# Performance work log

Measured on AMD Instinct MI355X. Metric: run time of the kernel, lower is better.

The kernel has to match this reference:

```python
import jax, jax.numpy as jnp
import numpy as np

B, S, H = 1, 4096, 2048
HQ, HKV, D = 8, 4, 256
WIN = 1024          # sliding window
SOFTCAP = 50.0      # attn logit softcapping
EPS = 1e-6          # rms_norm_eps
ROPE_THETA = 10000.0


def setup_inputs() -> dict:
    key = jax.random.key(0)
    ks = jax.random.split(key, 6)
    hidden_states = jax.random.normal(ks[0], (B, S, H), dtype=jnp.float32)
    # RoPE cos/sin tables, shape [B, S, D]
    inv_freq = 1.0 / (ROPE_THETA ** (jnp.arange(0, D, 2, dtype=jnp.float32) / D))
    pos = jnp.arange(S, dtype=jnp.float32)
    freqs = pos[:, None] * inv_freq[None, :]          # [S, D/2]
    emb = jnp.concatenate([freqs, freqs], axis=-1)    # [S, D]
    cos = jnp.broadcast_to(jnp.cos(emb)[None], (B, S, D)).astype(jnp.float32)
    sin = jnp.broadcast_to(jnp.sin(emb)[None], (B, S, D)).astype(jnp.float32)
    qpos = jnp.arange(S)[:, None]
    kpos = jnp.arange(S)[None, :]
    diff = qpos - kpos
    allowed = (diff >= 0) & (diff < WIN)
    attention_mask = jnp.where(allowed, 0.0, -1e9).astype(jnp.float32)[None, None]
    attention_mask = jnp.broadcast_to(attention_mask, (B, 1, S, S))
    w_scale = 0.02
    Wq = jax.random.normal(ks[1], (HQ * D, H), dtype=jnp.float32) * w_scale
    Wk = jax.random.normal(ks[2], (HKV * D, H), dtype=jnp.float32) * w_scale
    Wv = jax.random.normal(ks[3], (HKV * D, H), dtype=jnp.float32) * w_scale
    Wo = jax.random.normal(ks[4], (H, HQ * D), dtype=jnp.float32) * w_scale
    q_norm_w = jnp.ones((D,), dtype=jnp.float32)
    k_norm_w = jnp.ones((D,), dtype=jnp.float32)
    return {"hidden_states": hidden_states, "cos": cos, "sin": sin,
            "attention_mask": attention_mask, "Wq": Wq, "Wk": Wk, "Wv": Wv,
            "Wo": Wo, "q_norm_w": q_norm_w, "k_norm_w": k_norm_w}


def _rms_norm(x, weight=None):
    # Gemma4 RMSNorm in fp32: x * rsqrt(mean(x^2) + eps) [* weight]
    ms = jnp.mean(x * x, axis=-1, keepdims=True) + EPS
    y = x * jax.lax.rsqrt(ms)
    return y * weight if weight is not None else y


def _rope(x, cos, sin):
    # x: [B,S,Hn,D]; cos/sin: [B,S,D] -> unsqueeze at dim 2
    x1, x2 = jnp.split(x, 2, axis=-1)
    rot = jnp.concatenate([-x2, x1], axis=-1)
    return x * cos[:, :, None, :] + rot * sin[:, :, None, :]


def reference(hidden_states, cos, sin, attention_mask, Wq, Wk, Wv, Wo, q_norm_w, k_norm_w):
    n_rep = HQ // HKV
    q = (hidden_states @ Wq.T).reshape(B, S, HQ, D)     # [B,S,HQ,D]
    q = _rms_norm(q, q_norm_w)
    q = _rope(q, cos, sin).transpose(0, 2, 1, 3)        # [B,HQ,S,D]
    k = (hidden_states @ Wk.T).reshape(B, S, HKV, D)
    k = _rms_norm(k, k_norm_w)
    k = _rope(k, cos, sin).transpose(0, 2, 1, 3)        # [B,HKV,S,D]
    v = (hidden_states @ Wv.T).reshape(B, S, HKV, D)
    v = _rms_norm(v).transpose(0, 2, 1, 3)              # [B,HKV,S,D]
    # repeat_kv (GQA)
    k = jnp.repeat(k, n_rep, axis=1)                    # [B,HQ,S,D]
    v = jnp.repeat(v, n_rep, axis=1)
    scores = jnp.einsum('bhqd,bhkd->bhqk', q, k)        # scaling = 1.0
    scores = jnp.tanh(scores / SOFTCAP) * SOFTCAP       # softcap
    scores = scores + attention_mask
    attn = jax.nn.softmax(scores.astype(jnp.float32), axis=-1).astype(q.dtype)
    out = jnp.einsum('bhqk,bhkd->bhqd', attn, v)        # [B,HQ,S,D]
    out = out.transpose(0, 2, 1, 3).reshape(B, S, HQ * D)
    return out @ Wo.T                                   # [B,S,H]
```

## Files before the change

kernel.cpp:

```cpp
#include <hip/hip_runtime.h>

#define S_LEN 4096
#define HID   2048
#define NHQ   8
#define NKV   4
#define DHEAD 256
#define WIN   1024

typedef __attribute__((ext_vector_type(4))) float     floatx4;
typedef __attribute__((ext_vector_type(8))) _Float16  halfx8;
typedef __attribute__((ext_vector_type(8))) __bf16    bf16x8;

__device__ __forceinline__ unsigned short f2h(float f){
  union { _Float16 h; unsigned short u; } cv; cv.h = (_Float16)f; return cv.u;
}
__device__ __forceinline__ float h2f(unsigned short u){
  union { unsigned short u; _Float16 h; } cv; cv.u = u; return (float)cv.h;
}
__device__ __forceinline__ unsigned short f2bf(float f){
  unsigned int u = __float_as_uint(f);
  u += 0x7FFFu + ((u >> 16) & 1u);
  return (unsigned short)(u >> 16);
}

__device__ __forceinline__ void gld_lds16(const void* g, void* l){
  __builtin_amdgcn_global_load_lds((const __attribute__((address_space(1))) void*)g,
                                   (__attribute__((address_space(3))) void*)l, 16, 0, 0);
}

__global__ __launch_bounds__(256) void cvt_all(const float* __restrict__ hs,
                                               const float* __restrict__ Wq,
                                               const float* __restrict__ Wk,
                                               const float* __restrict__ Wv,
                                               const float* __restrict__ Wo,
                                               unsigned short* __restrict__ h_h,
                                               unsigned short* __restrict__ w_qkv,
                                               unsigned short* __restrict__ wo){
  int bid = blockIdx.x;
  const float* src;
  unsigned short* dst;
  size_t i;
  if (bid < 8192){
    i = ((size_t)bid * 256 + threadIdx.x) * 4;
    src = hs + i; dst = h_h + i;
  } else if (bid < 16384){
    i = ((size_t)(bid - 8192) * 256 + threadIdx.x) * 4;
    int row = (int)(i >> 11), col = (int)(i & 2047);
    src = ((row < 2048) ? (Wq + ((size_t)row << 11))
         : (row < 3072) ? (Wk + ((size_t)(row - 2048) << 11))
                        : (Wv + ((size_t)(row - 3072) << 11))) + col;
    dst = w_qkv + i;
  } else {
    i = ((size_t)(bid - 16384) * 256 + threadIdx.x) * 4;
    src = Wo + i; dst = wo + i;
  }
  float4 v = *(const float4*)src;
  *(ushort4*)dst = make_ushort4(f2h(v.x), f2h(v.y), f2h(v.z), f2h(v.w));
}

template<int OUT_F32>
__global__ __launch_bounds__(256, 2) void gemm_ht(const unsigned short* __restrict__ A,
                                                  const unsigned short* __restrict__ B,
                                                  void* __restrict__ Cv,
                                                  int ldC, int K){
  __shared__ __align__(16) unsigned short As[128 * 32];
  __shared__ __align__(16) unsigned short Bs[128 * 32];
  const int t = threadIdx.x, w = t >> 6, lane = t & 63;
  const int quad = lane >> 4, l15 = lane & 15;
  const int l2 = lane >> 2, g8 = (lane & 3) * 8;
  const int wm = w >> 1, wn = w & 1;
  const int bm0 = blockIdx.y * 128, bn0 = blockIdx.x * 128;

  const floatx4 zf = {0.f, 0.f, 0.f, 0.f};
  floatx4 acc[4][4];
#pragma unroll
  for (int mi = 0; mi < 4; ++mi)
#pragma unroll
    for (int ni = 0; ni < 4; ++ni) acc[mi][ni] = zf;

  for (int k0 = 0; k0 < K; k0 += 32){
#pragma unroll
    for (int j = 0; j < 2; ++j){
      int ch  = j * 4 + w;
      int row = ch * 16 + l2;
      gld_lds16(A + (size_t)(bm0 + row) * K + k0 + g8, &As[ch * 512]);
      gld_lds16(B + (size_t)(bn0 + row) * K + k0 + g8, &Bs[ch * 512]);
    }
    __syncthreads();
    halfx8 af[4], bf[4];
#pragma unroll
    for (int mi = 0; mi < 4; ++mi) af[mi] = *(const halfx8*)&As[(wm*64 + mi*16 + l15)*32 + quad*8];
#pragma unroll
    for (int ni = 0; ni < 4; ++ni) bf[ni] = *(const halfx8*)&Bs[(wn*64 + ni*16 + l15)*32 + quad*8];
#pragma unroll
    for (int mi = 0; mi < 4; ++mi)
#pragma unroll
      for (int ni = 0; ni < 4; ++ni)
        acc[mi][ni] = __builtin_amdgcn_mfma_f32_16x16x32_f16(af[mi], bf[ni], acc[mi][ni], 0, 0, 0);
    __syncthreads();
  }
#pragma unroll
  for (int mi = 0; mi < 4; ++mi)
#pragma unroll
    for (int ni = 0; ni < 4; ++ni)
#pragma unroll
      for (int r = 0; r < 4; ++r){
        int m = bm0 + wm*64 + mi*16 + quad*4 + r;
        int n = bn0 + wn*64 + ni*16 + l15;
        float v = acc[mi][ni][r];
        if (OUT_F32) ((float*)Cv)[(size_t)m * ldC + n] = v;
        else         ((unsigned short*)Cv)[(size_t)m * ldC + n] = f2h(v);
      }
}

__global__ __launch_bounds__(256) void qkv_post(const unsigned short* __restrict__ qkvh,
                                                const float* __restrict__ cosb,
                                                const float* __restrict__ sinb,
                                                const float* __restrict__ qnw,
                                                const float* __restrict__ knw,
                                                unsigned short* __restrict__ Qf,
                                                unsigned short* __restrict__ Kf,
                                                unsigned short* __restrict__ Vf){
  int gw   = blockIdx.x * 4 + (threadIdx.x >> 6);
  int lane = threadIdx.x & 63;
  int hh = gw & 15, s = gw >> 4;
  int colbase = (hh < 8) ? hh * 256 : (hh < 12 ? 2048 + (hh - 8) * 256 : 3072 + (hh - 12) * 256);

  ushort4 raw = *(const ushort4*)(qkvh + (size_t)s * 4096 + colbase + lane * 4);
  float x0 = h2f(raw.x), x1 = h2f(raw.y), x2 = h2f(raw.z), x3 = h2f(raw.w);
  float ss = x0*x0 + x1*x1 + x2*x2 + x3*x3;
#pragma unroll
  for (int off = 32; off; off >>= 1) ss += __shfl_xor(ss, off);
  float inv = rsqrtf(ss * (1.0f / 256.0f) + 1e-6f);

  if (hh < 12){
    const float* wp = (hh < 8) ? qnw : knw;
    float4 wv = *(const float4*)(wp + lane * 4);
    float y[4] = { x0*inv*wv.x, x1*inv*wv.y, x2*inv*wv.z, x3*inv*wv.w };
    float4 cv = *(const float4*)(cosb + (size_t)s * 256 + lane * 4);
    float4 sv = *(const float4*)(sinb + (size_t)s * 256 + lane * 4);
    float cj[4] = {cv.x, cv.y, cv.z, cv.w};
    float sj[4] = {sv.x, sv.y, sv.z, sv.w};
    unsigned short oh[4];
#pragma unroll
    for (int j = 0; j < 4; ++j){
      float oth = __shfl_xor(y[j], 32);
      float rot = (lane < 32) ? -oth : oth;
      oh[j] = f2h(y[j] * cj[j] + rot * sj[j]);
    }
    ushort4 r = make_ushort4(oh[0], oh[1], oh[2], oh[3]);
    if (hh < 8) *(ushort4*)(Qf + (size_t)(hh       * S_LEN + s) * DHEAD + lane * 4) = r;
    else        *(ushort4*)(Kf + (size_t)((hh - 8) * S_LEN + s) * DHEAD + lane * 4) = r;
  } else {
    ushort4 r = make_ushort4(f2bf(x0*inv), f2bf(x1*inv), f2bf(x2*inv), f2bf(x3*inv));
    *(ushort4*)(Vf + (size_t)((hh - 12) * S_LEN + s) * DHEAD + lane * 4) = r;
  }
}

__global__ __launch_bounds__(256) void transpose_v(const unsigned short* __restrict__ v,
                                                   unsigned short* __restrict__ vt){
  __shared__ unsigned short tile[64][68];
  int kv = blockIdx.z, d0 = blockIdx.x * 64, s0 = blockIdx.y * 64;
  int t = threadIdx.x;
  int r = t >> 4, c4 = (t & 15) * 4;
#pragma unroll
  for (int i = 0; i < 4; ++i){
    int row = r + i * 16;
    ushort4 xx = *(const ushort4*)(v + (size_t)(kv * S_LEN + s0 + row) * DHEAD + d0 + c4);
    tile[row][c4] = xx.x; tile[row][c4+1] = xx.y; tile[row][c4+2] = xx.z; tile[row][c4+3] = xx.w;
  }
  __syncthreads();
#pragma unroll
  for (int i = 0; i < 4; ++i){
    int dr = r + i * 16;
    ushort4 yy = make_ushort4(tile[c4][dr], tile[c4+1][dr], tile[c4+2][dr], tile[c4+3][dr]);
    *(ushort4*)(vt + (size_t)(kv * DHEAD + d0 + dr) * S_LEN + s0 + c4) = yy;
  }
}

__global__ __launch_bounds__(256, 2) void attn_win(const unsigned short* __restrict__ Qg,
                                                   const unsigned short* __restrict__ Kg,
                                                   const unsigned short* __restrict__ Vt,
                                                   unsigned short* __restrict__ Og){
  __shared__ __align__(16) unsigned short Ks[2][8 * 32 * 32];
  __shared__ __align__(16) unsigned short Vts[2][256 * 32];
  __shared__ __align__(16) unsigned short Pb[4][16 * 40];

  const int bid = blockIdx.x;
  const int h = bid & 7, kv = h >> 1;
  const int q0 = (bid >> 3) * 64;
  const int t = threadIdx.x, w = t >> 6, lane = t & 63;
  const int quad = lane >> 4, l15 = lane & 15;
  const int l2 = lane >> 2;
  const int gsw = (((lane & 3) ^ ((l2 >> 1) & 3)) << 3);
  const int qsw = ((quad ^ ((l15 >> 1) & 3)) << 3);
  const int qw0 = q0 + w * 16;

  halfx8 qf[8];
#pragma unroll
  for (int c = 0; c < 8; ++c)
    qf[c] = *(const halfx8*)(Qg + (size_t)(h * S_LEN + qw0 + l15) * DHEAD + c*32 + quad*8);

  const floatx4 zf = {0.f, 0.f, 0.f, 0.f};
  floatx4 oacc[16];
#pragma unroll
  for (int dt = 0; dt < 16; ++dt) oacc[dt] = zf;
  float l_part[4] = {0.f, 0.f, 0.f, 0.f};

  int kt_lo = q0 / 32 - 32; if (kt_lo < 0) kt_lo = 0;
  int kt_hi = q0 / 32 + 1;

  const size_t kbase = (size_t)kv * S_LEN * DHEAD;
  const size_t vbase = (size_t)kv * DHEAD * S_LEN;

#define STAGE(KT, B)                                                              \
  {                                                                               \
    const int key0_ = (KT) * 32;                                                  \
    _Pragma("unroll")                                                             \
    for (int j = 0; j < 4; ++j){                                                  \
      int ch = j * 4 + w;                                                         \
      int krow = (ch & 1) * 16 + l2;                                              \
      int cb = ch >> 1;                                                           \
      gld_lds16(Kg + kbase + (size_t)(key0_ + krow) * DHEAD + cb * 32 + gsw,      \
                &Ks[B][ch * 512]);                                                \
      int drow = ch * 16 + l2;                                                    \
      gld_lds16(Vt + vbase + (size_t)drow * S_LEN + key0_ + gsw,                  \
                &Vts[B][ch * 512]);                                               \
    }                                                                             \
  }

  STAGE(kt_lo, 0);

  for (int kt = kt_lo; kt <= kt_hi; ++kt){
    const int cur = (kt - kt_lo) & 1;
    __syncthreads();
    if (kt < kt_hi) STAGE(kt + 1, cur ^ 1);

    const int key0 = kt * 32;
    if (key0 <= qw0 + 15 && key0 + 31 >= qw0 - (WIN - 1)){
      floatx4 sc[2];
      sc[0] = zf; sc[1] = zf;
      __builtin_amdgcn_s_setprio(1);
#pragma unroll
      for (int c = 0; c < 8; ++c){
#pragma unroll
        for (int nt = 0; nt < 2; ++nt){
          halfx8 kf = *(const halfx8*)&Ks[cur][c * 1024 + (nt*16 + l15) * 32 + qsw];
          sc[nt] = __builtin_amdgcn_mfma_f32_16x16x32_f16(qf[c], kf, sc[nt], 0, 0, 0);
        }
      }
      __builtin_amdgcn_s_setprio(0);
      const bool tfull = (key0 + 31 <= qw0) && (qw0 + 15 - key0 < WIN);
#pragma unroll
      for (int nt = 0; nt < 2; ++nt)
#pragma unroll
        for (int r = 0; r < 4; ++r){
          float v = sc[nt][r];
          float e  = __builtin_amdgcn_exp2f(v * 0.0577078016f);
          float tt = __builtin_amdgcn_rcpf(e + 1.0f);
          float p  = __builtin_amdgcn_exp2f(fmaf(tt, -144.26950408f, 28.8539008f));
          if (!tfull){
            int qi = qw0 + quad*4 + r;
            int ki = key0 + nt*16 + l15;
            p = ((ki <= qi) && (qi - ki < WIN)) ? p : 0.0f;
          }
          l_part[r] += p;
          Pb[w][(quad*4 + r) * 40 + nt*16 + l15] = f2bf(p);
        }
      bf16x8 pf = *(const bf16x8*)&Pb[w][l15 * 40 + quad * 8];
      __builtin_amdgcn_s_setprio(1);
#pragma unroll
      for (int dt = 0; dt < 16; ++dt){
        bf16x8 vf = *(const bf16x8*)&Vts[cur][(dt*16 + l15) * 32 + qsw];
        oacc[dt] = __builtin_amdgcn_mfma_f32_16x16x32_bf16(pf, vf, oacc[dt], 0, 0, 0);
      }
      __builtin_amdgcn_s_setprio(0);
    }
  }
#undef STAGE

#pragma unroll
  for (int r = 0; r < 4; ++r){
    float l = l_part[r];
    l += __shfl_xor(l, 1);
    l += __shfl_xor(l, 2);
    l += __shfl_xor(l, 4);
    l += __shfl_xor(l, 8);
    float rl = 1.0f / l;
    int srow = qw0 + quad*4 + r;
#pragma unroll
    for (int dt = 0; dt < 16; ++dt)
      Og[(size_t)srow * (NHQ * DHEAD) + h * DHEAD + dt*16 + l15] = f2h(oacc[dt][r] * rl);
  }
}

extern "C" void kernel_launch(void* const* d_in, const int* in_sizes, int n_in,
                              void* d_out, int out_size, void* d_ws, size_t ws_size,
                              hipStream_t stream){
  const float* hs   = (const float*)d_in[0];
  const float* cosb = (const float*)d_in[1];
  const float* sinb = (const float*)d_in[2];
  const float* Wq   = (const float*)d_in[4];
  const float* Wk   = (const float*)d_in[5];
  const float* Wv   = (const float*)d_in[6];
  const float* Wo   = (const float*)d_in[7];
  const float* qnw  = (const float*)d_in[8];
  const float* knw  = (const float*)d_in[9];
  float* out = (float*)d_out;

  const size_t MB = 1024ull * 1024ull;
  char* ws = (char*)d_ws;
  unsigned short* h_h   = (unsigned short*)(ws);
  unsigned short* w_qkv = (unsigned short*)(ws + 16 * MB);
  unsigned short* wo    = (unsigned short*)(ws + 32 * MB);
  unsigned short* qkvh  = (unsigned short*)(ws + 40 * MB);
  unsigned short* Qf    = (unsigned short*)(ws);
  unsigned short* Kf    = (unsigned short*)(ws + 16 * MB);
  unsigned short* Vf    = (unsigned short*)(ws + 24 * MB);
  unsigned short* vt    = (unsigned short*)(ws + 40 * MB);
  unsigned short* ob    = (unsigned short*)(ws + 48 * MB);

  cvt_all<<<20480, 256, 0, stream>>>(hs, Wq, Wk, Wv, Wo, h_h, w_qkv, wo);

  gemm_ht<0><<<dim3(32, 32), 256, 0, stream>>>(h_h, w_qkv, qkvh, 4096, 2048);

  qkv_post<<<16384, 256, 0, stream>>>(qkvh, cosb, sinb, qnw, knw, Qf, Kf, Vf);
  transpose_v<<<dim3(4, 64, 4), 256, 0, stream>>>(Vf, vt);

  attn_win<<<512, 256, 0, stream>>>(Qf, Kf, vt, ob);

  gemm_ht<1><<<dim3(16, 32), 256, 0, stream>>>(ob, wo, out, 2048, 2048);
}
```

Measured before the change: 395.5 us.

## Replace QKV projection GEMM with 256x256 tile, 4-stage LDS pipelined kernel

Adds a dedicated QKV projection GEMM that uses 256x256 block tiles with 512 threads and a 4-deep ring of LDS stages. The stages are filled by direct global-to-LDS loads with a swizzled layout, and the block index is remapped. Each K step is split into two MFMA phases that interleave the A and B prefetches, using explicit waitcnt, barriers and setprio. The aim is to raise data reuse per tile and hide memory latency so the projection runs closer to MFMA peak. The cost is a much larger LDS footprint (128KB per block) and more register pressure, which may limit occupancy to one block per CU. The launch now issues only 256 blocks.

```diff
diff --git a/kernel.cpp b/kernel.cpp
--- a/kernel.cpp
+++ b/kernel.cpp
@@ -58,6 +58,112 @@
   *(ushort4*)dst = make_ushort4(f2h(v.x), f2h(v.y), f2h(v.z), f2h(v.w));
 }
 
+__global__ __launch_bounds__(512, 2) void gemm_qkv(const unsigned short* __restrict__ A,
+                                                   const unsigned short* __restrict__ B,
+                                                   unsigned short* __restrict__ C,
+                                                   int ldC, int K){
+  __shared__ __align__(16) unsigned short As[4][256 * 32];
+  __shared__ __align__(16) unsigned short Bs[4][256 * 32];
+  const int T = K >> 5;
+  const int t0 = threadIdx.x;
+  const int w = t0 >> 6, lane = t0 & 63;
+  const int wm = w >> 2, wn = w & 3;
+  const int quad = lane >> 4, l15 = lane & 15;
+  const int qsw8 = ((quad ^ ((l15 >> 1) & 3)) << 3);
+
+  const int srow   = t0 >> 2;
+  const int swcol8 = (((t0 & 3) ^ ((t0 >> 3) & 3)) << 3);
+  const int sldst  = srow * 32 + ((t0 & 3) << 3);
+
+  const int bid = blockIdx.x;
+  const int wg = (bid & 7) * 32 + (bid >> 3);
+  const int bm0 = (wg >> 4) * 256, bn0 = (wg & 15) * 256;
+
+  const unsigned short* a0 = A + (size_t)(bm0 +       srow) * K + swcol8;
+  const unsigned short* a1 = A + (size_t)(bm0 + 128 + srow) * K + swcol8;
+  const unsigned short* b0 = B + (size_t)(bn0 +       srow) * K + swcol8;
+  const unsigned short* b1 = B + (size_t)(bn0 + 128 + srow) * K + swcol8;
+
+#define STA(U) { const int sl_ = (U) & 3;                                   \
+    gld_lds16(a0 + (size_t)(U) * 32, &As[sl_][sldst]);                      \
+    gld_lds16(a1 + (size_t)(U) * 32, &As[sl_][4096 + sldst]); }
+#define STB(U) { const int sl_ = (U) & 3;                                   \
+    gld_lds16(b0 + (size_t)(U) * 32, &Bs[sl_][sldst]);                      \
+    gld_lds16(b1 + (size_t)(U) * 32, &Bs[sl_][4096 + sldst]); }
+
+  STA(0) STB(0) STA(1) STB(1) STA(2) STB(2)
+  asm volatile("s_waitcnt vmcnt(8)" ::: "memory");
+  __builtin_amdgcn_s_barrier();
+  __builtin_amdgcn_sched_barrier(0);
+
+  const floatx4 zf = {0.f, 0.f, 0.f, 0.f};
+  floatx4 acc[8][4];
+#pragma unroll
+  for (int mi = 0; mi < 8; ++mi)
+#pragma unroll
+    for (int ni = 0; ni < 4; ++ni) acc[mi][ni] = zf;
+
+  const int arow = wm * 128 + l15;
+  const int brow = wn * 64  + l15;
+
+  for (int t = 0; t < T; ++t){
+    const int s = t & 3;
+    const unsigned short* Ap = &As[s][0];
+    const unsigned short* Bp = &Bs[s][0];
+    halfx8 af[4], bf[4];
+
+#pragma unroll
+    for (int mi = 0; mi < 4; ++mi) af[mi] = *(const halfx8*)&Ap[(arow + mi*16) * 32 + qsw8];
+#pragma unroll
+    for (int ni = 0; ni < 4; ++ni) bf[ni] = *(const halfx8*)&Bp[(brow + ni*16) * 32 + qsw8];
+    if (t + 3 < T) STA(t + 3)
+    __builtin_amdgcn_s_barrier();
+    asm volatile("s_waitcnt lgkmcnt(0)" ::: "memory");
+    __builtin_amdgcn_sched_barrier(0);
+    __builtin_amdgcn_s_setprio(1);
+#pragma unroll
+    for (int mi = 0; mi < 4; ++mi)
+#pragma unroll
+      for (int ni = 0; ni < 4; ++ni)
+        acc[mi][ni] = __builtin_amdgcn_mfma_f32_16x16x32_f16(af[mi], bf[ni], acc[mi][ni], 0, 0, 0);
+    __builtin_amdgcn_s_setprio(0);
+    __builtin_amdgcn_s_barrier();
+    __builtin_amdgcn_sched_barrier(0);
+
+#pragma unroll
+    for (int mi = 0; mi < 4; ++mi) af[mi] = *(const halfx8*)&Ap[(arow + 64 + mi*16) * 32 + qsw8];
+    if (t + 3 < T) STB(t + 3)
+    __builtin_amdgcn_s_barrier();
+    asm volatile("s_waitcnt lgkmcnt(0)" ::: "memory");
+    __builtin_amdgcn_sched_barrier(0);
+    __builtin_amdgcn_s_setprio(1);
+#pragma unroll
+    for (int mi = 0; mi < 4; ++mi)
+#pragma unroll
+      for (int ni = 0; ni < 4; ++ni)
+        acc[4 + mi][ni] = __builtin_amdgcn_mfma_f32_16x16x32_f16(af[mi], bf[ni], acc[4 + mi][ni], 0, 0, 0);
+    __builtin_amdgcn_s_setprio(0);
+    if (t < T - 3)       { asm volatile("s_waitcnt vmcnt(8)" ::: "memory"); }
+    else if (t == T - 3) { asm volatile("s_waitcnt vmcnt(4)" ::: "memory"); }
+    else if (t == T - 2) { asm volatile("s_waitcnt vmcnt(0)" ::: "memory"); }
+    __builtin_amdgcn_s_barrier();
+    __builtin_amdgcn_sched_barrier(0);
+  }
+#undef STA
+#undef STB
+
+#pragma unroll
+  for (int mi = 0; mi < 8; ++mi)
+#pragma unroll
+    for (int ni = 0; ni < 4; ++ni)
+#pragma unroll
+      for (int r = 0; r < 4; ++r){
+        int m = bm0 + wm*128 + (mi >> 2)*64 + (mi & 3)*16 + quad*4 + r;
+        int n = bn0 + wn*64 + ni*16 + l15;
+        C[(size_t)m * ldC + n] = f2h(acc[mi][ni][r]);
+      }
+}
+
 template<int OUT_F32>
 __global__ __launch_bounds__(256, 2) void gemm_ht(const unsigned short* __restrict__ A,
                                                   const unsigned short* __restrict__ B,
@@ -322,7 +428,7 @@
 
   cvt_all<<<20480, 256, 0, stream>>>(hs, Wq, Wk, Wv, Wo, h_h, w_qkv, wo);
 
-  gemm_ht<0><<<dim3(32, 32), 256, 0, stream>>>(h_h, w_qkv, qkvh, 4096, 2048);
+  gemm_qkv<<<256, 512, 0, stream>>>(h_h, w_qkv, qkvh, 4096, 2048);
 
   qkv_post<<<16384, 256, 0, stream>>>(qkvh, cosb, sinb, qnw, knw, Qf, Kf, Vf);
   transpose_v<<<dim3(4, 64, 4), 256, 0, stream>>>(Vf, vt);
```

After: 387.9 us. No clear change (-1.9%).

## Triple-buffer GEMM with vmcnt waits, LDS swizzle, XCD remap; use counted waits in attention

Applied to the files above, without the earlier changes.

Rewrites the GEMM as a three-stage LDS pipeline. Loads are issued two tiles ahead, and explicit s_waitcnt vmcnt plus raw barriers replace the full __syncthreads. The GEMM also XOR-swizzles LDS columns to reduce bank conflicts, remaps block IDs across XCDs for cache locality, and raises occupancy hints. The attention kernel replaces its syncthreads with counted vmcnt waits and an extra trailing barrier so prefetch overlaps compute. The price is more LDS per block and fragile hand-counted wait values that must match the exact number of outstanding loads.

```diff
diff --git a/kernel.cpp b/kernel.cpp
--- a/kernel.cpp
+++ b/kernel.cpp
@@ -59,17 +59,39 @@
 }
 
 template<int OUT_F32>
-__global__ __launch_bounds__(256, 2) void gemm_ht(const unsigned short* __restrict__ A,
-                                                  const unsigned short* __restrict__ B,
-                                                  void* __restrict__ Cv,
-                                                  int ldC, int K){
-  __shared__ __align__(16) unsigned short As[128 * 32];
-  __shared__ __align__(16) unsigned short Bs[128 * 32];
-  const int t = threadIdx.x, w = t >> 6, lane = t & 63;
+__global__ __launch_bounds__(256, 3) void gemm_cnt(const unsigned short* __restrict__ A,
+                                                   const unsigned short* __restrict__ B,
+                                                   void* __restrict__ Cv,
+                                                   int ldC, int K, int nx){
+  __shared__ __align__(16) unsigned short As[3][128 * 32];
+  __shared__ __align__(16) unsigned short Bs[3][128 * 32];
+  const int T = K >> 5;
+  const int t0 = threadIdx.x, w = t0 >> 6, lane = t0 & 63;
+  const int wm = w >> 1, wn = w & 1;
   const int quad = lane >> 4, l15 = lane & 15;
-  const int l2 = lane >> 2, g8 = (lane & 3) * 8;
-  const int wm = w >> 1, wn = w & 1;
-  const int bm0 = blockIdx.y * 128, bn0 = blockIdx.x * 128;
+  const int qsw8 = ((quad ^ ((l15 >> 1) & 3)) << 3);
+
+  const int nwg = (int)gridDim.x;
+  const int wg = ((int)blockIdx.x & 7) * (nwg >> 3) + ((int)blockIdx.x >> 3);
+  const int by = wg / nx, bx = wg - by * nx;
+  const int bm0 = by * 128, bn0 = bx * 128;
+
+  const int sr = t0 >> 2;
+  const int swc8 = (((t0 & 3) ^ ((t0 >> 3) & 3)) << 3);
+  const int ldst = sr * 32 + ((t0 & 3) << 3);
+  const unsigned short* aG = A + (size_t)(bm0 + sr) * K + swc8;
+  const unsigned short* bG = B + (size_t)(bn0 + sr) * K + swc8;
+
+#define STAGE(U, SL) {                                                        \
+    gld_lds16(aG + (size_t)(U) * 32,                  &As[SL][ldst]);         \
+    gld_lds16(aG + (size_t)(U) * 32 + (size_t)64 * K, &As[SL][2048 + ldst]);  \
+    gld_lds16(bG + (size_t)(U) * 32,                  &Bs[SL][ldst]);         \
+    gld_lds16(bG + (size_t)(U) * 32 + (size_t)64 * K, &Bs[SL][2048 + ldst]); }
+
+  STAGE(0, 0)
+  STAGE(1, 1)
+  asm volatile("s_waitcnt vmcnt(4)" ::: "memory");
+  __builtin_amdgcn_s_barrier();
 
   const floatx4 zf = {0.f, 0.f, 0.f, 0.f};
   floatx4 acc[4][4];
@@ -78,27 +100,33 @@
 #pragma unroll
     for (int ni = 0; ni < 4; ++ni) acc[mi][ni] = zf;
 
-  for (int k0 = 0; k0 < K; k0 += 32){
-#pragma unroll
-    for (int j = 0; j < 2; ++j){
-      int ch  = j * 4 + w;
-      int row = ch * 16 + l2;
-      gld_lds16(A + (size_t)(bm0 + row) * K + k0 + g8, &As[ch * 512]);
-      gld_lds16(B + (size_t)(bn0 + row) * K + k0 + g8, &Bs[ch * 512]);
+  int sl = 0;
+  for (int t = 0; t < T; ++t){
+    const unsigned short* Ap = &As[sl][0];
+    const unsigned short* Bp = &Bs[sl][0];
+    halfx8 af[4], bf[4];
+#pragma unroll
+    for (int mi = 0; mi < 4; ++mi) af[mi] = *(const halfx8*)&Ap[(wm*64 + mi*16 + l15)*32 + qsw8];
+#pragma unroll
+    for (int ni = 0; ni < 4; ++ni) bf[ni] = *(const halfx8*)&Bp[(wn*64 + ni*16 + l15)*32 + qsw8];
+    if (t + 2 < T){
+      const int sn = sl ? sl - 1 : 2;
+      STAGE(t + 2, sn)
     }
-    __syncthreads();
-    halfx8 af[4], bf[4];
-#pragma unroll
-    for (int mi = 0; mi < 4; ++mi) af[mi] = *(const halfx8*)&As[(wm*64 + mi*16 + l15)*32 + quad*8];
-#pragma unroll
-    for (int ni = 0; ni < 4; ++ni) bf[ni] = *(const halfx8*)&Bs[(wn*64 + ni*16 + l15)*32 + quad*8];
+    __builtin_amdgcn_s_setprio(1);
 #pragma unroll
     for (int mi = 0; mi < 4; ++mi)
 #pragma unroll
       for (int ni = 0; ni < 4; ++ni)
         acc[mi][ni] = __builtin_amdgcn_mfma_f32_16x16x32_f16(af[mi], bf[ni], acc[mi][ni], 0, 0, 0);
-    __syncthreads();
-  }
+    __builtin_amdgcn_s_setprio(0);
+    if (t < T - 2)       { asm volatile("s_waitcnt vmcnt(4)" ::: "memory"); }
+    else if (t == T - 2) { asm volatile("s_waitcnt vmcnt(0)" ::: "memory"); }
+    __builtin_amdgcn_s_barrier();
+    sl = (sl == 2) ? 0 : sl + 1;
+  }
+#undef STAGE
+
 #pragma unroll
   for (int mi = 0; mi < 4; ++mi)
 #pragma unroll
@@ -233,8 +261,13 @@
 
   for (int kt = kt_lo; kt <= kt_hi; ++kt){
     const int cur = (kt - kt_lo) & 1;
-    __syncthreads();
-    if (kt < kt_hi) STAGE(kt + 1, cur ^ 1);
+    if (kt < kt_hi){
+      STAGE(kt + 1, cur ^ 1);
+      asm volatile("s_waitcnt vmcnt(8)" ::: "memory");
+    } else {
+      asm volatile("s_waitcnt vmcnt(0)" ::: "memory");
+    }
+    __builtin_amdgcn_s_barrier();
 
     const int key0 = kt * 32;
     if (key0 <= qw0 + 15 && key0 + 31 >= qw0 - (WIN - 1)){
@@ -276,6 +309,7 @@
       }
       __builtin_amdgcn_s_setprio(0);
     }
+    __builtin_amdgcn_s_barrier();
   }
 #undef STAGE
 
@@ -322,12 +356,12 @@
 
   cvt_all<<<20480, 256, 0, stream>>>(hs, Wq, Wk, Wv, Wo, h_h, w_qkv, wo);
 
-  gemm_ht<0><<<dim3(32, 32), 256, 0, stream>>>(h_h, w_qkv, qkvh, 4096, 2048);
+  gemm_cnt<0><<<1024, 256, 0, stream>>>(h_h, w_qkv, qkvh, 4096, 2048, 32);
 
   qkv_post<<<16384, 256, 0, stream>>>(qkvh, cosb, sinb, qnw, knw, Qf, Kf, Vf);
   transpose_v<<<dim3(4, 64, 4), 256, 0, stream>>>(Vf, vt);
 
   attn_win<<<512, 256, 0, stream>>>(Qf, Kf, vt, ob);
 
-  gemm_ht<1><<<dim3(16, 32), 256, 0, stream>>>(ob, wo, out, 2048, 2048);
-}
+  gemm_cnt<1><<<512, 256, 0, stream>>>(ob, wo, out, 2048, 2048, 16);
+}
```

New measurement: 404.9 us. +2.4%, slower.
